# Optimization experiments

Measured on AMD Instinct MI355X. Metric: run time of the kernel, lower is better.

The kernel has to match this reference:

```python
import jax, jax.numpy as jnp
import numpy as np

T, B, F, P = 1024, 2048, 11, 256
KAPPA_MAX = 0.1
N_GRID = 100


def setup_inputs() -> dict:
    key = jax.random.key(0)
    k1, k2, k3, k4, k5 = jax.random.split(key, 5)
    aidx = jax.random.randint(k1, (T, B), 0, 2)
    actions = jax.nn.one_hot(aidx, 2, dtype=jnp.float32)            # (T,B,2) one-hot choice
    rewards = jax.random.bernoulli(k2, 0.5, (T, B, 2)).astype(jnp.float32)
    cd_cur = jax.random.uniform(k3, (T, B, 1), minval=-0.1, maxval=0.1)
    cd_next = jax.random.uniform(k4, (T, B, 1), minval=-0.1, maxval=0.1)
    meta = jnp.zeros((T, B, 4), dtype=jnp.float32)                  # timestep/trial/block/experiment (unused)
    pid = jax.random.randint(k5, (B,), 0, P).astype(jnp.float32)
    pid_feat = jnp.broadcast_to(pid[None, :, None], (T, B, 1))
    inputs = jnp.concatenate([actions, rewards, cd_cur, cd_next, meta, pid_feat], axis=-1)
    inputs = inputs[:, None]                                        # (T, 1, B, 11)
    return {
        "inputs": inputs,
        "beta_raw": jnp.zeros((P,), dtype=jnp.float32),
        "sigma_raw": jnp.zeros((P,), dtype=jnp.float32),
    }


def reference(inputs, beta_raw, sigma_raw):
    p_mu = jnp.linspace(0.0, 1.0, N_GRID)                           # (100,)
    x = jnp.nan_to_num(inputs[:, 0])                                # (T, B, 11)
    pid = x[0, :, -1].astype(jnp.int32)                             # (B,)
    beta = jnp.clip(jax.nn.softplus(beta_raw) + 1.0, 1.0, 25.0)[pid]    # (B,)
    sigma = jnp.clip(jax.nn.sigmoid(sigma_raw) * 0.09 + 0.01, 0.01, 0.1)[pid]  # (B,)
    inv_s = 1.0 / (sigma * jnp.sqrt(2.0))

    def ncdf(v, mean):
        return 0.5 * (1.0 + jax.lax.erf((v - mean) * inv_s))

    def state_beliefs(cd):
        u = ncdf(0.0, cd)
        v = ncdf(-KAPPA_MAX, cd)
        w = ncdf(KAPPA_MAX, cd)
        denom = jnp.maximum(w - v, 1e-10)
        pi_0 = jnp.clip((u - v) / denom, 0.0, 1.0)
        pi_1 = jnp.clip((w - u) / denom, 0.0, 1.0)
        return pi_0, pi_1

    def step(belief, x_t):
        acts = x_t[:, :2]
        rews = x_t[:, 2:4]
        cd_current = x_t[:, 4]
        cd_next = x_t[:, 5]
        had_choice = acts.sum(-1) > 0
        action_idx = jnp.argmax(acts, axis=-1)
        reward_scalar = (rews * acts).sum(-1)
        pi_0, pi_1 = state_beliefs(cd_current)
        r = jnp.where(action_idx == 0, reward_scalar, 1.0 - reward_scalar)
        q_0 = pi_1 * r + pi_0 * (1.0 - r)
        q_1 = (2.0 * r - 1.0) * (pi_0 - pi_1)
        update = q_1[:, None] * p_mu + q_0[:, None]                 # (B, 100)
        update = jnp.where(had_choice[:, None], update, 1.0)
        belief = jnp.maximum(belief * update, 1e-30)
        belief_norm = belief / belief.sum(-1, keepdims=True)
        E_mu = (belief_norm * p_mu).sum(-1)                         # (B,)
        pi_0n, pi_1n = state_beliefs(cd_next)
        v_a0 = (pi_0n - pi_1n) * E_mu + pi_1n
        v_a1 = (pi_1n - pi_0n) * E_mu + pi_0n
        logits_t = beta[:, None] * jnp.stack([v_a0, v_a1], axis=-1)  # (B, 2)
        return belief, logits_t

    belief0 = jnp.ones((x.shape[1], N_GRID), dtype=x.dtype)
    belief, logits = jax.lax.scan(step, belief0, x)                 # logits: (T, B, 2)
    logits = logits[:, None]                                        # (T, 1, B, 2)
    return logits, belief
```

## Files before the change

kernel.cpp:

```cpp
#include <hip/hip_runtime.h>
#include <math.h>

#define TT  1024
#define BB  2048
#define FF  11
#define PP  256
#define NG  100
#define NCH 32
#define LCH (TT / NCH)
#define JJ  4

typedef float f32x2 __attribute__((ext_vector_type(2)));
typedef float f32x4u __attribute__((ext_vector_type(4), aligned(4)));
typedef float f32x2u __attribute__((ext_vector_type(2), aligned(4)));

__device__ __forceinline__ float nz(float v) { return (v != v) ? 0.f : v; }

__device__ __forceinline__ float erf_fast(float x) {
    float ax = fabsf(x);
    float t  = __builtin_amdgcn_rcpf(fmaf(0.3275911f, ax, 1.f));
    float y  = fmaf(fmaf(fmaf(fmaf(1.061405429f, t, -1.453152027f), t,
                              1.421413741f), t, -0.284496736f), t, 0.254829592f);
    y *= t;
    float r = fmaf(-y, __expf(-ax * ax), 1.f);
    return copysignf(r, x);
}

__device__ __forceinline__ float4 q_from_rec(
    float a0, float a1, float r0, float r1, float cdc, float cdn,
    float beta, float inv_s)
{
    float u = 0.5f * (1.f + erf_fast((0.0f  - cdc) * inv_s));
    float v = 0.5f * (1.f + erf_fast((-0.1f - cdc) * inv_s));
    float w = 0.5f * (1.f + erf_fast((0.1f  - cdc) * inv_s));
    float inv = 1.f / fmaxf(w - v, 1e-10f);
    float pi0 = fminf(fmaxf((u - v) * inv, 0.f), 1.f);
    float pi1 = fminf(fmaxf((w - u) * inv, 0.f), 1.f);

    u = 0.5f * (1.f + erf_fast((0.0f  - cdn) * inv_s));
    v = 0.5f * (1.f + erf_fast((-0.1f - cdn) * inv_s));
    w = 0.5f * (1.f + erf_fast((0.1f  - cdn) * inv_s));
    inv = 1.f / fmaxf(w - v, 1e-10f);
    float pi0n = fminf(fmaxf((u - v) * inv, 0.f), 1.f);
    float pi1n = fminf(fmaxf((w - u) * inv, 0.f), 1.f);

    float rs = r0 * a0 + r1 * a1;
    float r  = (a0 >= a1) ? rs : 1.f - rs;
    float q0 = pi1 * r + pi0 * (1.f - r);
    float q1 = (2.f * r - 1.f) * (pi0 - pi1);
    if (!((a0 + a1) > 0.f)) { q0 = 1.f; q1 = 0.f; }
    return make_float4(q0, q1, beta * pi1n, beta * pi0n);
}


__global__ __launch_bounds__(256, 4) void phaseAq_kernel(
    const float* __restrict__ x, const float* __restrict__ beta_raw,
    const float* __restrict__ sigma_raw, float4* __restrict__ QC,
    float* __restrict__ UC)
{
    __shared__ float2 sq[4][64];
    const int lane = threadIdx.x & 63;
    const int wib  = threadIdx.x >> 6;
    const int W    = blockIdx.x * 4 + wib;
    const int wg   = W & 255;
    const int c    = W >> 8;
    const int g    = lane & 7;
    const int sl   = lane >> 3;
    const int b    = wg * 8 + g;
    const int t0   = c * LCH;
    float2* sqw = sq[wib];

    f32x4u r4[4];
    f32x2u r2[4];
    #pragma unroll
    for (int r = 0; r < 4; ++r) {
        const float* rec = x + (size_t)(t0 + 8 * r + sl) * (BB * FF) + b * FF;
        r4[r] = *(const f32x4u*)rec;
        r2[r] = *(const f32x2u*)(rec + 4);
    }

    int pid = (int)nz(x[(size_t)b * FF + 10]);
    pid = pid < 0 ? 0 : (pid > PP - 1 ? PP - 1 : pid);
    float br = beta_raw[pid];
    float sr = sigma_raw[pid];
    float sp   = fmaxf(br, 0.f) + log1pf(__expf(-fabsf(br)));
    float beta = fminf(fmaxf(sp + 1.f, 1.f), 25.f);
    float sig  = fminf(fmaxf(__builtin_amdgcn_rcpf(1.f + __expf(-sr)) * 0.09f + 0.01f,
                             0.01f), 0.1f);
    float inv_s = 1.f / (sig * 1.41421356237309505f);

    f32x2 p[7];
    #pragma unroll
    for (int k = 0; k < 7; ++k)
        p[k] = (f32x2){ (float)(sl + 16 * k)     * (1.f / 99.f),
                        (float)(sl + 16 * k + 8) * (1.f / 99.f) };

    f32x2 U[7];
    #pragma unroll
    for (int k = 0; k < 7; ++k) U[k] = (f32x2){1.f, 1.f};

    #pragma unroll
    for (int r = 0; r < 4; ++r) {
        float a0 = nz(r4[r].x), a1 = nz(r4[r].y), r0 = nz(r4[r].z),
              r1 = nz(r4[r].w), dc = nz(r2[r].x), dn = nz(r2[r].y);
        float4 qc = q_from_rec(a0, a1, r0, r1, dc, dn, beta, inv_s);
        QC[(size_t)(t0 + 8 * r + sl) * BB + b] = qc;

        sqw[sl * 8 + g] = make_float2(qc.x, qc.y);
        __builtin_amdgcn_wave_barrier();
        #pragma unroll
        for (int j = 0; j < 8; ++j) {
            float2 qj = sqw[j * 8 + g];
            f32x2 qx = { qj.x, qj.x }, qy = { qj.y, qj.y };
            #pragma unroll
            for (int k = 0; k < 7; ++k) {
                f32x2 u = qy * p[k] + qx;
                U[k] *= u;
            }
        }
        __builtin_amdgcn_wave_barrier();
    }

    float* dst = UC + (size_t)c * (NG * BB) + b;
    #pragma unroll
    for (int k = 0; k < 6; ++k) {
        dst[(size_t)(sl + 16 * k) * BB]     = U[k].x;
        dst[(size_t)(sl + 16 * k + 8) * BB] = U[k].y;
    }
    if (sl < 4) dst[(size_t)(sl + 96) * BB] = U[6].x;
}

__global__ __launch_bounds__(256) void phaseB_kernel(
    const float* __restrict__ UC, float* __restrict__ BE)
{
    const int flat = blockIdx.x * 256 + threadIdx.x;
    float be = 1.f;
    #pragma unroll
    for (int c = 0; c < NCH; ++c) {
        BE[(size_t)c * (BB * NG) + flat] = be;
        float u = UC[(size_t)c * (BB * NG) + flat];
        be = fmaxf(be * u, 1e-30f);
    }
}

__global__ __launch_bounds__(256) void phaseC_kernel(
    const float4* __restrict__ QC, const float* __restrict__ BE,
    float* __restrict__ out)
{
    const int lane = threadIdx.x & 63;
    const int wib  = threadIdx.x >> 6;
    const int W    = blockIdx.x * 4 + wib;
    const int wg   = W & 255;
    const int c    = W >> 8;
    const int sl   = lane & 7;
    const int g    = lane >> 3;
    const int b    = wg * 8 + g;
    const int t0   = c * LCH;

    f32x2 p[7];
    #pragma unroll
    for (int k = 0; k < 7; ++k)
        p[k] = (f32x2){ (float)(sl + 16 * k)     * (1.f / 99.f),
                        (float)(sl + 16 * k + 8) * (1.f / 99.f) };
    const f32x2 clA = { 1e-30f, 1e-30f };
    const f32x2 cl6 = { (sl < 4) ? 1e-30f : 0.f, 0.f };

    const float* ebase = BE + (size_t)c * (BB * NG) + b;
    f32x2 be[7];
    #pragma unroll
    for (int k = 0; k < 6; ++k)
        be[k] = (f32x2){ ebase[(size_t)(sl + 16 * k) * BB],
                         ebase[(size_t)(sl + 16 * k + 8) * BB] };
    be[6] = (f32x2){ (sl < 4) ? ebase[(size_t)(sl + 96) * BB] : 0.f, 0.f };

    const char* QCb = (const char*)QC;
    char* outb = (char*)out;
    unsigned off  = ((unsigned)t0 * BB + (unsigned)b) * 16u;
    unsigned soff = ((unsigned)t0 * (2 * BB) + 2 * (unsigned)b) * 4u;

    float4 pre[JJ];
    #pragma unroll
    for (int j = 0; j < JJ; ++j)
        pre[j] = *(const float4*)(QCb + (off + (unsigned)j * (BB * 16u)));
    off += JJ * (BB * 16u);

    for (int tt = 0; tt < LCH; tt += JJ) {
        float S[JJ], Sp[JJ], Zv[JJ], Wv[JJ];
        #pragma unroll
        for (int j = 0; j < JJ; ++j) {
            float4 q = pre[j];
            pre[j] = *(const float4*)(QCb + (off + (unsigned)j * (BB * 16u)));
            f32x2 qx = { q.x, q.x }, qy = { q.y, q.y };
            #pragma unroll
            for (int k = 0; k < 7; ++k) {
                f32x2 u = qy * p[k] + qx;
                be[k] = __builtin_elementwise_max(be[k] * u,
                                                  (k == 6) ? cl6 : clA);
            }
            f32x2 sA = ((be[0] + be[1]) + (be[2] + be[3]))
                     + ((be[4] + be[5]) + be[6]);
            S[j] = sA.x + sA.y;
            f32x2 a1 = be[0] * p[0], a2 = be[1] * p[1];
            a1 = be[2] * p[2] + a1;  a2 = be[3] * p[3] + a2;
            a1 = be[4] * p[4] + a1;  a2 = be[5] * p[5] + a2;
            a1 = be[6] * p[6] + a1;
            f32x2 aa = a1 + a2;
            Sp[j] = aa.x + aa.y;
            Zv[j] = q.z;
            Wv[j] = q.w;
        }
        off += JJ * (BB * 16u);
        #pragma unroll
        for (int j = 0; j < JJ; ++j) {
            float st = S[j], sr = Sp[j];
            {
                int t;
                t = __builtin_amdgcn_update_dpp(0, __float_as_int(st), 0xB1, 0xF, 0xF, true);
                st += __int_as_float(t);
                t = __builtin_amdgcn_update_dpp(0, __float_as_int(sr), 0xB1, 0xF, 0xF, true);
                sr += __int_as_float(t);
                t = __builtin_amdgcn_update_dpp(0, __float_as_int(st), 0x4E, 0xF, 0xF, true);
                st += __int_as_float(t);
                t = __builtin_amdgcn_update_dpp(0, __float_as_int(sr), 0x4E, 0xF, 0xF, true);
                sr += __int_as_float(t);
                t = __builtin_amdgcn_update_dpp(0, __float_as_int(st), 0x141, 0xF, 0xF, true);
                st += __int_as_float(t);
                t = __builtin_amdgcn_update_dpp(0, __float_as_int(sr), 0x141, 0xF, 0xF, true);
                sr += __int_as_float(t);
            }
            float E  = sr * __builtin_amdgcn_rcpf(st);
            float A  = Wv[j] - Zv[j];
            float l0 = fmaf(A, E, Zv[j]);
            float l1 = fmaf(-A, E, Wv[j]);
            if (sl == 0)
                *(float2*)(outb + (soff + (unsigned)j * (2 * BB * 4u))) =
                    make_float2(l0, l1);
        }
        soff += JJ * (2 * BB * 4u);
    }

    if (c == NCH - 1) {
        float* bel = out + (size_t)TT * BB * 2 + (size_t)b * NG;
        #pragma unroll
        for (int k = 0; k < 6; ++k) {
            bel[sl + 16 * k]     = be[k].x;
            bel[sl + 16 * k + 8] = be[k].y;
        }
        if (sl < 4) bel[sl + 96] = be[6].x;
    }
}

extern "C" void kernel_launch(void* const* d_in, const int* in_sizes, int n_in,
                              void* d_out, int out_size, void* d_ws, size_t ws_size,
                              hipStream_t stream)
{
    const float* x         = (const float*)d_in[0];
    const float* beta_raw  = (const float*)d_in[1];
    const float* sigma_raw = (const float*)d_in[2];
    float* out = (float*)d_out;

    char* ws = (char*)d_ws;
    float4* QC = (float4*)ws;
    float*  UC = (float*)(ws + (size_t)TT * BB * 16);
    float*  BE = (float*)(ws + (size_t)TT * BB * 16 + (size_t)NCH * BB * NG * 4);

    phaseAq_kernel<<<(BB / 8) * NCH / 4, 256, 0, stream>>>(x, beta_raw, sigma_raw, QC, UC);
    phaseB_kernel<<<(BB * NG) / 256, 256, 0, stream>>>(UC, BE);
    phaseC_kernel<<<(BB / 8) * NCH / 4, 256, 0, stream>>>(QC, BE, out);
}
```

Before: 195.8 us.

## Fuse three phases into one cooperative kernel and recompute Q instead of storing it

Replaces the three separate kernels with one cooperative kernel that uses grid-wide syncs between the chunk-product, prefix-scan and replay phases. Q coefficients are recomputed from the raw inputs in the replay phase, so the QC intermediate buffer is gone. UC/BE now use a paired float2 layout, and each block handles four time chunks with a double-buffered input prefetch. This removes launch gaps and the QC write/read traffic. In exchange it pays for recomputing the erf math, uses fewer waves (a 512-block grid), serializes the phase-B scan onto 56*BB threads, and adds two grid barriers. If the cooperative launch fails, it falls back to three launches.

After: 467.8 us. 139% more time.

```diff
diff --git a/kernel.cpp b/kernel.cpp
--- a/kernel.cpp
+++ b/kernel.cpp
@@ -1,4 +1,5 @@
 #include <hip/hip_runtime.h>
+#include <hip/hip_cooperative_groups.h>
 #include <math.h>
 
 #define TT  1024
@@ -8,7 +9,9 @@
 #define NG  100
 #define NCH 32
 #define LCH (TT / NCH)
-#define JJ  4
+#define GRID 512
+
+namespace cg = cooperative_groups;
 
 typedef float f32x2 __attribute__((ext_vector_type(2)));
 typedef float f32x4u __attribute__((ext_vector_type(4), aligned(4)));
@@ -52,33 +55,10 @@
     return make_float4(q0, q1, beta * pi1n, beta * pi0n);
 }
 
-
-__global__ __launch_bounds__(256, 4) void phaseAq_kernel(
+__device__ __forceinline__ float2 participant(
     const float* __restrict__ x, const float* __restrict__ beta_raw,
-    const float* __restrict__ sigma_raw, float4* __restrict__ QC,
-    float* __restrict__ UC)
+    const float* __restrict__ sigma_raw, int b)
 {
-    __shared__ float2 sq[4][64];
-    const int lane = threadIdx.x & 63;
-    const int wib  = threadIdx.x >> 6;
-    const int W    = blockIdx.x * 4 + wib;
-    const int wg   = W & 255;
-    const int c    = W >> 8;
-    const int g    = lane & 7;
-    const int sl   = lane >> 3;
-    const int b    = wg * 8 + g;
-    const int t0   = c * LCH;
-    float2* sqw = sq[wib];
-
-    f32x4u r4[4];
-    f32x2u r2[4];
-    #pragma unroll
-    for (int r = 0; r < 4; ++r) {
-        const float* rec = x + (size_t)(t0 + 8 * r + sl) * (BB * FF) + b * FF;
-        r4[r] = *(const f32x4u*)rec;
-        r2[r] = *(const f32x2u*)(rec + 4);
-    }
-
     int pid = (int)nz(x[(size_t)b * FF + 10]);
     pid = pid < 0 ? 0 : (pid > PP - 1 ? PP - 1 : pid);
     float br = beta_raw[pid];
@@ -87,166 +67,220 @@
     float beta = fminf(fmaxf(sp + 1.f, 1.f), 25.f);
     float sig  = fminf(fmaxf(__builtin_amdgcn_rcpf(1.f + __expf(-sr)) * 0.09f + 0.01f,
                              0.01f), 0.1f);
-    float inv_s = 1.f / (sig * 1.41421356237309505f);
-
-    f32x2 p[7];
-    #pragma unroll
-    for (int k = 0; k < 7; ++k)
-        p[k] = (f32x2){ (float)(sl + 16 * k)     * (1.f / 99.f),
-                        (float)(sl + 16 * k + 8) * (1.f / 99.f) };
-
-    f32x2 U[7];
-    #pragma unroll
-    for (int k = 0; k < 7; ++k) U[k] = (f32x2){1.f, 1.f};
-
-    #pragma unroll
-    for (int r = 0; r < 4; ++r) {
-        float a0 = nz(r4[r].x), a1 = nz(r4[r].y), r0 = nz(r4[r].z),
-              r1 = nz(r4[r].w), dc = nz(r2[r].x), dn = nz(r2[r].y);
-        float4 qc = q_from_rec(a0, a1, r0, r1, dc, dn, beta, inv_s);
-        QC[(size_t)(t0 + 8 * r + sl) * BB + b] = qc;
-
-        sqw[sl * 8 + g] = make_float2(qc.x, qc.y);
-        __builtin_amdgcn_wave_barrier();
-        #pragma unroll
-        for (int j = 0; j < 8; ++j) {
-            float2 qj = sqw[j * 8 + g];
-            f32x2 qx = { qj.x, qj.x }, qy = { qj.y, qj.y };
-            #pragma unroll
-            for (int k = 0; k < 7; ++k) {
-                f32x2 u = qy * p[k] + qx;
-                U[k] *= u;
-            }
-        }
-        __builtin_amdgcn_wave_barrier();
-    }
-
-    float* dst = UC + (size_t)c * (NG * BB) + b;
-    #pragma unroll
-    for (int k = 0; k < 6; ++k) {
-        dst[(size_t)(sl + 16 * k) * BB]     = U[k].x;
-        dst[(size_t)(sl + 16 * k + 8) * BB] = U[k].y;
-    }
-    if (sl < 4) dst[(size_t)(sl + 96) * BB] = U[6].x;
-}
-
-__global__ __launch_bounds__(256) void phaseB_kernel(
-    const float* __restrict__ UC, float* __restrict__ BE)
+    return make_float2(beta, 1.f / (sig * 1.41421356237309505f));
+}
+
+__global__ __launch_bounds__(256, 2) void fused_kernel(
+    const float* __restrict__ x, const float* __restrict__ beta_raw,
+    const float* __restrict__ sigma_raw, float2* __restrict__ UC2,
+    float2* __restrict__ BE2, float* __restrict__ out, int phase)
 {
-    const int flat = blockIdx.x * 256 + threadIdx.x;
-    float be = 1.f;
-    #pragma unroll
-    for (int c = 0; c < NCH; ++c) {
-        BE[(size_t)c * (BB * NG) + flat] = be;
-        float u = UC[(size_t)c * (BB * NG) + flat];
-        be = fmaxf(be * u, 1e-30f);
-    }
-}
-
-__global__ __launch_bounds__(256) void phaseC_kernel(
-    const float4* __restrict__ QC, const float* __restrict__ BE,
-    float* __restrict__ out)
-{
+    __shared__ float2 sq[4][64];
+    __shared__ float4 tile[4][8][8];
     const int lane = threadIdx.x & 63;
     const int wib  = threadIdx.x >> 6;
-    const int W    = blockIdx.x * 4 + wib;
-    const int wg   = W & 255;
-    const int c    = W >> 8;
-    const int sl   = lane & 7;
-    const int g    = lane >> 3;
-    const int b    = wg * 8 + g;
-    const int t0   = c * LCH;
-
-    f32x2 p[7];
-    #pragma unroll
-    for (int k = 0; k < 7; ++k)
-        p[k] = (f32x2){ (float)(sl + 16 * k)     * (1.f / 99.f),
-                        (float)(sl + 16 * k + 8) * (1.f / 99.f) };
-    const f32x2 clA = { 1e-30f, 1e-30f };
-    const f32x2 cl6 = { (sl < 4) ? 1e-30f : 0.f, 0.f };
-
-    const float* ebase = BE + (size_t)c * (BB * NG) + b;
-    f32x2 be[7];
-    #pragma unroll
-    for (int k = 0; k < 6; ++k)
-        be[k] = (f32x2){ ebase[(size_t)(sl + 16 * k) * BB],
-                         ebase[(size_t)(sl + 16 * k + 8) * BB] };
-    be[6] = (f32x2){ (sl < 4) ? ebase[(size_t)(sl + 96) * BB] : 0.f, 0.f };
-
-    const char* QCb = (const char*)QC;
-    char* outb = (char*)out;
-    unsigned off  = ((unsigned)t0 * BB + (unsigned)b) * 16u;
-    unsigned soff = ((unsigned)t0 * (2 * BB) + 2 * (unsigned)b) * 4u;
-
-    float4 pre[JJ];
-    #pragma unroll
-    for (int j = 0; j < JJ; ++j)
-        pre[j] = *(const float4*)(QCb + (off + (unsigned)j * (BB * 16u)));
-    off += JJ * (BB * 16u);
-
-    for (int tt = 0; tt < LCH; tt += JJ) {
-        float S[JJ], Sp[JJ], Zv[JJ], Wv[JJ];
+    const int wv   = blockIdx.x * 4 + wib;
+    const int wg   = wv & 255;
+    const int q    = wv >> 8;
+    float2* sqw = sq[wib];
+
+    if (phase <= 0) {
+        const int g1  = lane & 7;
+        const int sl1 = lane >> 3;
+        const int b1  = wg * 8 + g1;
+        const float2 pr = participant(x, beta_raw, sigma_raw, b1);
+        const float beta = pr.x, inv_s = pr.y;
+
+        f32x2 p1[7];
         #pragma unroll
-        for (int j = 0; j < JJ; ++j) {
-            float4 q = pre[j];
-            pre[j] = *(const float4*)(QCb + (off + (unsigned)j * (BB * 16u)));
-            f32x2 qx = { q.x, q.x }, qy = { q.y, q.y };
-            #pragma unroll
-            for (int k = 0; k < 7; ++k) {
-                f32x2 u = qy * p[k] + qx;
-                be[k] = __builtin_elementwise_max(be[k] * u,
-                                                  (k == 6) ? cl6 : clA);
-            }
-            f32x2 sA = ((be[0] + be[1]) + (be[2] + be[3]))
-                     + ((be[4] + be[5]) + be[6]);
-            S[j] = sA.x + sA.y;
-            f32x2 a1 = be[0] * p[0], a2 = be[1] * p[1];
-            a1 = be[2] * p[2] + a1;  a2 = be[3] * p[3] + a2;
-            a1 = be[4] * p[4] + a1;  a2 = be[5] * p[5] + a2;
-            a1 = be[6] * p[6] + a1;
-            f32x2 aa = a1 + a2;
-            Sp[j] = aa.x + aa.y;
-            Zv[j] = q.z;
-            Wv[j] = q.w;
+        for (int k = 0; k < 7; ++k)
+            p1[k] = (f32x2){ (float)(sl1 + 16 * k)     * (1.f / 99.f),
+                             (float)(sl1 + 16 * k + 8) * (1.f / 99.f) };
+
+        f32x4u r4[2][4];
+        f32x2u r2[2][4];
+        {
+            const int t0 = q * LCH;
+            #pragma unroll
+            for (int r = 0; r < 4; ++r) {
+                const float* rec = x + (size_t)(t0 + 8 * r + sl1) * (BB * FF) + b1 * FF;
+                r4[0][r] = *(const f32x4u*)rec;
+                r2[0][r] = *(const f32x2u*)(rec + 4);
+            }
         }
-        off += JJ * (BB * 16u);
         #pragma unroll
-        for (int j = 0; j < JJ; ++j) {
-            float st = S[j], sr = Sp[j];
+        for (int ti = 0; ti < 4; ++ti) {
+            if (ti < 3) {
+                const int t0n = (q + (ti + 1) * 8) * LCH;
+                #pragma unroll
+                for (int r = 0; r < 4; ++r) {
+                    const float* rec = x + (size_t)(t0n + 8 * r + sl1) * (BB * FF) + b1 * FF;
+                    r4[(ti + 1) & 1][r] = *(const f32x4u*)rec;
+                    r2[(ti + 1) & 1][r] = *(const f32x2u*)(rec + 4);
+                }
+            }
+            const int c = q + ti * 8;
+            f32x2 U[7];
+            #pragma unroll
+            for (int k = 0; k < 7; ++k) U[k] = (f32x2){1.f, 1.f};
+
+            #pragma unroll
+            for (int r = 0; r < 4; ++r) {
+                float a0 = nz(r4[ti & 1][r].x), a1 = nz(r4[ti & 1][r].y),
+                      r0 = nz(r4[ti & 1][r].z), r1 = nz(r4[ti & 1][r].w),
+                      dc = nz(r2[ti & 1][r].x), dn = nz(r2[ti & 1][r].y);
+                float4 qc = q_from_rec(a0, a1, r0, r1, dc, dn, beta, inv_s);
+                sqw[sl1 * 8 + g1] = make_float2(qc.x, qc.y);
+                __builtin_amdgcn_wave_barrier();
+                #pragma unroll
+                for (int j = 0; j < 8; ++j) {
+                    float2 qj = sqw[j * 8 + g1];
+                    f32x2 qx = { qj.x, qj.x }, qy = { qj.y, qj.y };
+                    #pragma unroll
+                    for (int k = 0; k < 7; ++k) {
+                        f32x2 uu = qy * p1[k] + qx;
+                        U[k] *= uu;
+                    }
+                }
+                __builtin_amdgcn_wave_barrier();
+            }
+            #pragma unroll
+            for (int k = 0; k < 7; ++k)
+                UC2[((size_t)c * 56 + k * 8 + sl1) * BB + b1] =
+                    make_float2(U[k].x, U[k].y);
+        }
+    }
+
+    if (phase == -1) { __threadfence(); cg::this_grid().sync(); }
+
+    if (phase == -1 || phase == 1) {
+        const int tid = blockIdx.x * 256 + threadIdx.x;
+        if (tid < 56 * BB) {
+            f32x2 be = {1.f, 1.f};
+            const f32x2 cl = {1e-30f, 1e-30f};
+            for (int c = 0; c < NCH; ++c) {
+                BE2[(size_t)c * (56 * BB) + tid] = make_float2(be.x, be.y);
+                float2 Uv = UC2[(size_t)c * (56 * BB) + tid];
+                f32x2 uu = { Uv.x, Uv.y };
+                be = __builtin_elementwise_max(be * uu, cl);
+            }
+        }
+    }
+
+    if (phase == -1) { __threadfence(); cg::this_grid().sync(); }
+
+    if (phase == -1 || phase == 2) {
+        const int sl  = lane & 7;
+        const int g   = lane >> 3;
+        const int b   = wg * 8 + g;
+        const int g1  = lane & 7;
+        const int sl1 = lane >> 3;
+        const int b1  = wg * 8 + g1;
+        const float2 pr = participant(x, beta_raw, sigma_raw, b1);
+        const float beta = pr.x, inv_s = pr.y;
+
+        f32x2 p3[7];
+        #pragma unroll
+        for (int k = 0; k < 7; ++k)
+            p3[k] = (f32x2){ (float)(sl + 16 * k)     * (1.f / 99.f),
+                             (float)(sl + 16 * k + 8) * (1.f / 99.f) };
+        const f32x2 clA = { 1e-30f, 1e-30f };
+        const f32x2 cl6 = { (sl < 4) ? 1e-30f : 0.f, 0.f };
+
+        for (int ti = 0; ti < 4; ++ti) {
+            const int c  = q + ti * 8;
+            const int t0 = c * LCH;
+
+            f32x4u r4[4];
+            f32x2u r2[4];
+            #pragma unroll
+            for (int r = 0; r < 4; ++r) {
+                const float* rec = x + (size_t)(t0 + 8 * r + sl1) * (BB * FF) + b1 * FF;
+                r4[r] = *(const f32x4u*)rec;
+                r2[r] = *(const f32x2u*)(rec + 4);
+            }
+
+            f32x2 be[7];
+            #pragma unroll
+            for (int k = 0; k < 6; ++k) {
+                float2 v = BE2[((size_t)c * 56 + k * 8 + sl) * BB + b];
+                be[k] = (f32x2){ v.x, v.y };
+            }
             {
-                int t;
-                t = __builtin_amdgcn_update_dpp(0, __float_as_int(st), 0xB1, 0xF, 0xF, true);
-                st += __int_as_float(t);
-                t = __builtin_amdgcn_update_dpp(0, __float_as_int(sr), 0xB1, 0xF, 0xF, true);
-                sr += __int_as_float(t);
-                t = __builtin_amdgcn_update_dpp(0, __float_as_int(st), 0x4E, 0xF, 0xF, true);
-                st += __int_as_float(t);
-                t = __builtin_amdgcn_update_dpp(0, __float_as_int(sr), 0x4E, 0xF, 0xF, true);
-                sr += __int_as_float(t);
-                t = __builtin_amdgcn_update_dpp(0, __float_as_int(st), 0x141, 0xF, 0xF, true);
-                st += __int_as_float(t);
-                t = __builtin_amdgcn_update_dpp(0, __float_as_int(sr), 0x141, 0xF, 0xF, true);
-                sr += __int_as_float(t);
-            }
-            float E  = sr * __builtin_amdgcn_rcpf(st);
-            float A  = Wv[j] - Zv[j];
-            float l0 = fmaf(A, E, Zv[j]);
-            float l1 = fmaf(-A, E, Wv[j]);
-            if (sl == 0)
-                *(float2*)(outb + (soff + (unsigned)j * (2 * BB * 4u))) =
-                    make_float2(l0, l1);
+                float2 v = BE2[((size_t)c * 56 + 6 * 8 + sl) * BB + b];
+                be[6] = (f32x2){ (sl < 4) ? v.x : 0.f, 0.f };
+            }
+
+            #pragma unroll
+            for (int r = 0; r < 4; ++r) {
+                float a0 = nz(r4[r].x), a1 = nz(r4[r].y), r0 = nz(r4[r].z),
+                      r1 = nz(r4[r].w), dc = nz(r2[r].x), dn = nz(r2[r].y);
+                float4 qc = q_from_rec(a0, a1, r0, r1, dc, dn, beta, inv_s);
+                tile[wib][sl1][g1] = qc;
+                __builtin_amdgcn_wave_barrier();
+
+                float S[8], Sp[8], Zv[8], Wv[8];
+                #pragma unroll
+                for (int j = 0; j < 8; ++j) {
+                    float4 qf = tile[wib][j][g];
+                    f32x2 qx = { qf.x, qf.x }, qy = { qf.y, qf.y };
+                    #pragma unroll
+                    for (int k = 0; k < 7; ++k) {
+                        f32x2 uu = qy * p3[k] + qx;
+                        be[k] = __builtin_elementwise_max(be[k] * uu,
+                                                          (k == 6) ? cl6 : clA);
+                    }
+                    f32x2 sA = ((be[0] + be[1]) + (be[2] + be[3]))
+                             + ((be[4] + be[5]) + be[6]);
+                    S[j] = sA.x + sA.y;
+                    f32x2 a1v = be[0] * p3[0], a2v = be[1] * p3[1];
+                    a1v = be[2] * p3[2] + a1v;  a2v = be[3] * p3[3] + a2v;
+                    a1v = be[4] * p3[4] + a1v;  a2v = be[5] * p3[5] + a2v;
+                    a1v = be[6] * p3[6] + a1v;
+                    f32x2 aa = a1v + a2v;
+                    Sp[j] = aa.x + aa.y;
+                    Zv[j] = qf.z;
+                    Wv[j] = qf.w;
+                }
+                #pragma unroll
+                for (int j = 0; j < 8; ++j) {
+                    float st = S[j], sr = Sp[j];
+                    {
+                        int t;
+                        t = __builtin_amdgcn_update_dpp(0, __float_as_int(st), 0xB1, 0xF, 0xF, true);
+                        st += __int_as_float(t);
+                        t = __builtin_amdgcn_update_dpp(0, __float_as_int(sr), 0xB1, 0xF, 0xF, true);
+                        sr += __int_as_float(t);
+                        t = __builtin_amdgcn_update_dpp(0, __float_as_int(st), 0x4E, 0xF, 0xF, true);
+                        st += __int_as_float(t);
+                        t = __builtin_amdgcn_update_dpp(0, __float_as_int(sr), 0x4E, 0xF, 0xF, true);
+                        sr += __int_as_float(t);
+                        t = __builtin_amdgcn_update_dpp(0, __float_as_int(st), 0x141, 0xF, 0xF, true);
+                        st += __int_as_float(t);
+                        t = __builtin_amdgcn_update_dpp(0, __float_as_int(sr), 0x141, 0xF, 0xF, true);
+                        sr += __int_as_float(t);
+                    }
+                    float E  = sr * __builtin_amdgcn_rcpf(st);
+                    float A  = Wv[j] - Zv[j];
+                    float l0 = fmaf(A, E, Zv[j]);
+                    float l1 = fmaf(-A, E, Wv[j]);
+                    if (sl == 0)
+                        *(float2*)(out + (size_t)(t0 + 8 * r + j) * (2 * BB) + 2 * b) =
+                            make_float2(l0, l1);
+                }
+                __builtin_amdgcn_wave_barrier();
+            }
+
+            if (c == NCH - 1) {
+                float* bel = out + (size_t)TT * BB * 2 + (size_t)b * NG;
+                #pragma unroll
+                for (int k = 0; k < 6; ++k) {
+                    bel[sl + 16 * k]     = be[k].x;
+                    bel[sl + 16 * k + 8] = be[k].y;
+                }
+                if (sl < 4) bel[sl + 96] = be[6].x;
+            }
         }
-        soff += JJ * (2 * BB * 4u);
-    }
-
-    if (c == NCH - 1) {
-        float* bel = out + (size_t)TT * BB * 2 + (size_t)b * NG;
-        #pragma unroll
-        for (int k = 0; k < 6; ++k) {
-            bel[sl + 16 * k]     = be[k].x;
-            bel[sl + 16 * k + 8] = be[k].y;
-        }
-        if (sl < 4) bel[sl + 96] = be[6].x;
     }
 }
 
@@ -259,12 +293,19 @@
     const float* sigma_raw = (const float*)d_in[2];
     float* out = (float*)d_out;
 
-    char* ws = (char*)d_ws;
-    float4* QC = (float4*)ws;
-    float*  UC = (float*)(ws + (size_t)TT * BB * 16);
-    float*  BE = (float*)(ws + (size_t)TT * BB * 16 + (size_t)NCH * BB * NG * 4);
-
-    phaseAq_kernel<<<(BB / 8) * NCH / 4, 256, 0, stream>>>(x, beta_raw, sigma_raw, QC, UC);
-    phaseB_kernel<<<(BB * NG) / 256, 256, 0, stream>>>(UC, BE);
-    phaseC_kernel<<<(BB / 8) * NCH / 4, 256, 0, stream>>>(QC, BE, out);
-}
+    float2* UC2 = (float2*)d_ws;
+    float2* BE2 = (float2*)((char*)d_ws + (size_t)NCH * 56 * BB * 8);
+
+    int ph = -1;
+    void* kargs[] = { (void*)&x, (void*)&beta_raw, (void*)&sigma_raw,
+                      (void*)&UC2, (void*)&BE2, (void*)&out, (void*)&ph };
+    hipError_t e = hipLaunchCooperativeKernel(
+        reinterpret_cast<void*>(fused_kernel), dim3(GRID), dim3(256),
+        kargs, 0, stream);
+    if (e != hipSuccess) {
+        (void)hipGetLastError();
+        fused_kernel<<<GRID, 256, 0, stream>>>(x, beta_raw, sigma_raw, UC2, BE2, out, 0);
+        fused_kernel<<<GRID, 256, 0, stream>>>(x, beta_raw, sigma_raw, UC2, BE2, out, 1);
+        fused_kernel<<<GRID, 256, 0, stream>>>(x, beta_raw, sigma_raw, UC2, BE2, out, 2);
+    }
+}
```
